# Performance work log

Hardware: AMD Instinct MI355X
Metric: run time of the kernel (lower is better)

## Reference

```python
import jax, jax.numpy as jnp
import numpy as np


def setup_inputs() -> dict:
    key = jax.random.key(0)
    ks = jax.random.split(key, 5)
    B, S, D = 4, 2048, 1024
    return {
        "query": jax.random.normal(ks[0], (B, S, D), dtype=jnp.float32),
        "value": jax.random.normal(ks[1], (B, S, D), dtype=jnp.float32),
        "Wq": jax.random.normal(ks[2], (D, D), dtype=jnp.float32) * 0.02,
        "Wk": jax.random.normal(ks[3], (D, D), dtype=jnp.float32) * 0.02,
        "Wv": jax.random.normal(ks[4], (D, D), dtype=jnp.float32) * 0.02,
        "num_heads": 16,
    }


def reference(query, value, Wq, Wk, Wv, num_heads):
    B, S, D = query.shape
    H = num_heads
    d = D // H
    # torch Linear: x @ W.T (no bias)
    Q = (query @ Wq.T).reshape(B, S, H, d)
    K = (value @ Wk.T).reshape(B, S, H, d)
    V = (value @ Wv.T).reshape(B, S, H, d)
    # Source scales by sqrt(hidden_size), not sqrt(head_dim)
    scale = 1.0 / jnp.sqrt(jnp.asarray(D, dtype=query.dtype))
    att = jnp.einsum("bqhd,bkhd->bhqk", Q, K) * scale  # [B,H,S,S]
    att = jax.nn.softmax(att, axis=-1)
    out = jnp.einsum("bhqk,bkhd->bqhd", att, V)  # [B,S,H,d]
    return out.reshape(B, S, D)
```

## Files before the change

### kernel.cpp

```cpp
#include <hip/hip_runtime.h>
#include <stdint.h>


typedef __attribute__((ext_vector_type(8))) short short8;
typedef __attribute__((ext_vector_type(4))) short s16x4;
typedef __attribute__((ext_vector_type(4))) float f32x4;

__device__ __forceinline__ unsigned short bf16_rne(float f) {
  union { float f; uint32_t u; } c; c.f = f;
  uint32_t u = c.u;
  return (unsigned short)((u + 0x7fffu + ((u >> 16) & 1u)) >> 16);
}

__device__ __forceinline__ f32x4 mfma_bf16(short8 a, short8 b, f32x4 c) {
  return __builtin_amdgcn_mfma_f32_16x16x32_bf16(a, b, c, 0, 0, 0);
}

#if __has_builtin(__builtin_amdgcn_mfma_f32_16x16x16bf16_1k)
__device__ __forceinline__ f32x4 mfma16(s16x4 a, s16x4 b, f32x4 c) {
  return __builtin_amdgcn_mfma_f32_16x16x16bf16_1k(a, b, c, 0, 0, 0);
}
#else
__device__ __forceinline__ f32x4 mfma16(s16x4 a, s16x4 b, f32x4 c) {
  asm volatile("v_mfma_f32_16x16x16_bf16 %0, %1, %2, %0"
               : "+v"(c) : "v"(a), "v"(b));
  return c;
}
#endif

#if __has_builtin(__builtin_amdgcn_exp2f)
#define EXP2F(x) __builtin_amdgcn_exp2f(x)
#else
#define EXP2F(x) exp2f(x)
#endif

__device__ __forceinline__ s16x4 cvtpk4(f32x4 v) {
  union { int i[2]; s16x4 s; } u;
  asm("v_cvt_pk_bf16_f32 %0, %1, %2" : "=v"(u.i[0]) : "v"(v[0]), "v"(v[1]));
  asm("v_cvt_pk_bf16_f32 %0, %1, %2" : "=v"(u.i[1]) : "v"(v[2]), "v"(v[3]));
  return u.s;
}

__device__ __forceinline__ void gload_lds16(const void* g, void* l) {
  __builtin_amdgcn_global_load_lds(
      (const __attribute__((address_space(1))) void*)g,
      (__attribute__((address_space(3))) void*)l,
      16, 0, 0);
}

__global__ void cvt_all(const float* __restrict__ q, const float* __restrict__ v,
                        const float* __restrict__ wq, const float* __restrict__ wk,
                        const float* __restrict__ wv,
                        unsigned short* __restrict__ xb, unsigned short* __restrict__ yb,
                        unsigned short* __restrict__ wqb, unsigned short* __restrict__ wkb,
                        unsigned short* __restrict__ wvb) {
  int blk = blockIdx.x;
  const float* src; unsigned short* dst; int off; float scale = 1.0f;
  if (blk < 8192)       { src = q;  dst = xb;  off = blk; }
  else if (blk < 16384) { src = v;  dst = yb;  off = blk - 8192; }
  else if (blk < 17408) { src = wq; dst = wqb; off = blk - 16384; scale = 0.04508422f; }
  else if (blk < 18432) { src = wk; dst = wkb; off = blk - 17408; }
  else                  { src = wv; dst = wvb; off = blk - 18432; }
  int i = (off * 256 + threadIdx.x) * 4;
  float4 x = *reinterpret_cast<const float4*>(src + i);
  ushort4 o;
  o.x = bf16_rne(x.x * scale); o.y = bf16_rne(x.y * scale);
  o.z = bf16_rne(x.z * scale); o.w = bf16_rne(x.w * scale);
  *reinterpret_cast<ushort4*>(dst + i) = o;
}

#define PG_K 1024

__global__ __launch_bounds__(256) void proj_gemm3(
    const unsigned short* __restrict__ xb, const unsigned short* __restrict__ yb,
    const unsigned short* __restrict__ wqb, const unsigned short* __restrict__ wkb,
    const unsigned short* __restrict__ wvb,
    unsigned short* __restrict__ qb, unsigned short* __restrict__ kb,
    unsigned short* __restrict__ vtb) {
  __shared__ char sA[128 * 128];
  __shared__ char sB[128 * 128];
  const int z = blockIdx.z;
  const unsigned short* A = (z == 0) ? xb : yb;
  const unsigned short* W = (z == 0) ? wqb : ((z == 1) ? wkb : wvb);
  unsigned short* outp = (z == 0) ? qb : ((z == 1) ? kb : vtb);
  const int mode = (z == 2) ? 1 : 0;

  const int t = threadIdx.x;
  const int wid = t >> 6;
  const int lane = t & 63;
  const int l15 = lane & 15, k16 = lane >> 4;
  const int bm = blockIdx.x * 128, bn = blockIdx.y * 128;
  const int wr = (wid >> 1) * 64, wc = (wid & 1) * 64;

  f32x4 acc[4][4];
#pragma unroll
  for (int m = 0; m < 4; ++m)
#pragma unroll
    for (int n = 0; n < 4; ++n) acc[m][n] = f32x4{0.f, 0.f, 0.f, 0.f};

  const int srow0 = t >> 3;
  const int cs = ((t & 7) * 16) ^ ((srow0 & 7) << 4);
  const char* gAr = (const char*)A + (size_t)(bm + srow0) * 2048 + cs;
  const char* gBr = (const char*)W + (size_t)(bn + srow0) * 2048 + cs;
  char* lA = sA + t * 16;
  char* lB = sB + t * 16;

  int afo[4][2], bfo[4][2];
#pragma unroll
  for (int m = 0; m < 4; ++m) {
    int ra = wr + m * 16 + l15, swa = (ra & 7) << 4;
    int rb = wc + m * 16 + l15, swb = (rb & 7) << 4;
#pragma unroll
    for (int h = 0; h < 2; ++h) {
      afo[m][h] = ra * 128 + ((h * 64 + k16 * 16) ^ swa);
      bfo[m][h] = rb * 128 + ((h * 64 + k16 * 16) ^ swb);
    }
  }

  for (int ks = 0; ks < 16; ++ks) {
    const int koff = ks * 128;
#pragma unroll
    for (int j = 0; j < 4; ++j) {
      gload_lds16(gAr + (size_t)j * 32 * 2048 + koff, lA + j * 4096);
      gload_lds16(gBr + (size_t)j * 32 * 2048 + koff, lB + j * 4096);
    }
    __syncthreads();
    short8 af[4][2], bfr[4][2];
#pragma unroll
    for (int m = 0; m < 4; ++m)
#pragma unroll
      for (int h = 0; h < 2; ++h) {
        af[m][h] = *reinterpret_cast<const short8*>(sA + afo[m][h]);
        bfr[m][h] = *reinterpret_cast<const short8*>(sB + bfo[m][h]);
      }
#pragma unroll
    for (int h = 0; h < 2; ++h)
#pragma unroll
      for (int m = 0; m < 4; ++m)
#pragma unroll
        for (int n = 0; n < 4; ++n)
          acc[m][n] = mfma_bf16(af[m][h], bfr[n][h], acc[m][n]);
    __syncthreads();
  }

#pragma unroll
  for (int m = 0; m < 4; ++m) {
#pragma unroll
    for (int n = 0; n < 4; ++n) {
#pragma unroll
      for (int j = 0; j < 4; ++j) {
        int row = bm + wr + m * 16 + k16 * 4 + j;
        int col = bn + wc + n * 16 + l15;
        int b = row >> 11, s = row & 2047;
        int h = col >> 6, jd = col & 63;
        int idx = (mode == 0) ? (((b * 16 + h) * 2048 + s) * 64 + jd)
                              : (((b * 16 + h) * 64 + jd) * 2048 + s);
        outp[idx] = bf16_rne(acc[m][n][j]);
      }
    }
  }
}

__global__ __launch_bounds__(256) void attn_lds(
    const unsigned short* __restrict__ qb, const unsigned short* __restrict__ kb,
    const unsigned short* __restrict__ vtb, float* __restrict__ out) {
  __shared__ char sK[2][8192];
  __shared__ char sV[2][8192];
  const int t = threadIdx.x;
  const int wid = t >> 6, lane = t & 63;
  const int l15 = lane & 15, k16 = lane >> 4;
  const int S = 2048;
  const int bid = blockIdx.x;
  const int xcd = bid & 7, slot = bid >> 3;
  const int bh = xcd * 8 + (slot >> 4);
  const int q0 = (slot & 15) * 128 + wid * 32;

  const unsigned short* Kh = kb + (size_t)bh * S * 64;
  const unsigned short* Vh = vtb + (size_t)bh * 64 * S;

  const int off0 = t * 16;
  const int off1 = 4096 + t * 16;
  const char* pk0 = (const char*)Kh + (off0 ^ (((off0 >> 7) & 7) << 4));
  const char* pk1 = (const char*)Kh + (off1 ^ (((off1 >> 7) & 7) << 4));
  const int vr0 = off0 >> 7, vc0 = off0 & 127;
  const int vr1 = off1 >> 7, vc1 = off1 & 127;
  const char* pv0 = (const char*)Vh + vr0 * (S * 2) + (vc0 ^ ((vr0 & 7) << 4));
  const char* pv1 = (const char*)Vh + vr1 * (S * 2) + (vc1 ^ ((vr1 & 7) << 4));

  short8 qf[2][2];
#pragma unroll
  for (int qt = 0; qt < 2; ++qt) {
    const unsigned short* qrow =
        qb + ((size_t)bh * S + q0 + qt * 16 + l15) * 64 + k16 * 8;
    qf[qt][0] = *reinterpret_cast<const short8*>(qrow);
    qf[qt][1] = *reinterpret_cast<const short8*>(qrow + 32);
  }

  int kfo[4][2], vfo[4][4];
#pragma unroll
  for (int n = 0; n < 4; ++n) {
    int row = n * 16 + l15, sw = (row & 7) << 4;
    kfo[n][0] = row * 128 + ((k16 * 16) ^ sw);
    kfo[n][1] = row * 128 + ((64 + k16 * 16) ^ sw);
  }
#pragma unroll
  for (int np = 0; np < 4; ++np) {
    int dv = np * 16 + l15, sw = (dv & 7) << 4;
#pragma unroll
    for (int kt = 0; kt < 4; ++kt)
      vfo[np][kt] = dv * 128 + ((kt * 32 + k16 * 8) ^ sw);
  }

  {
    char* lk = &sK[0][wid * 1024];
    char* lv = &sV[0][wid * 1024];
    gload_lds16(pk0, lk); gload_lds16(pk1, lk + 4096);
    gload_lds16(pv0, lv); gload_lds16(pv1, lv + 4096);
    pk0 += 8192; pk1 += 8192; pv0 += 128; pv1 += 128;
  }
  __syncthreads();

  f32x4 o[2][4];
  f32x4 lsum[2];
#pragma unroll
  for (int qt = 0; qt < 2; ++qt) {
    lsum[qt] = f32x4{0.f, 0.f, 0.f, 0.f};
#pragma unroll
    for (int np = 0; np < 4; ++np) o[qt][np] = f32x4{0.f, 0.f, 0.f, 0.f};
  }

  for (int tt = 0; tt < 32; ++tt) {
    const char* bK = sK[tt & 1];
    const char* bV = sV[tt & 1];
    if (tt < 31) {
      char* nk = &sK[(tt + 1) & 1][wid * 1024];
      char* nv = &sV[(tt + 1) & 1][wid * 1024];
      gload_lds16(pk0, nk); gload_lds16(pk1, nk + 4096);
      gload_lds16(pv0, nv); gload_lds16(pv1, nv + 4096);
      pk0 += 8192; pk1 += 8192; pv0 += 128; pv1 += 128;
    }

    f32x4 sa[2][4];
    __builtin_amdgcn_s_setprio(1);
#pragma unroll
    for (int n = 0; n < 4; ++n) {
      short8 kf0 = *reinterpret_cast<const short8*>(bK + kfo[n][0]);
      short8 kf1 = *reinterpret_cast<const short8*>(bK + kfo[n][1]);
#pragma unroll
      for (int qt = 0; qt < 2; ++qt) {
        f32x4 a = f32x4{0.f, 0.f, 0.f, 0.f};
        a = mfma_bf16(kf0, qf[qt][0], a);
        a = mfma_bf16(kf1, qf[qt][1], a);
        sa[qt][n] = a;
      }
    }
    __builtin_amdgcn_s_setprio(0);
    s16x4 pf[2][4];
#pragma unroll
    for (int qt = 0; qt < 2; ++qt)
#pragma unroll
      for (int n = 0; n < 4; ++n) {
#pragma unroll
        for (int r = 0; r < 4; ++r) sa[qt][n][r] = EXP2F(sa[qt][n][r]);
        lsum[qt] += sa[qt][n];
        pf[qt][n] = cvtpk4(sa[qt][n]);
      }
    __builtin_amdgcn_s_setprio(1);
#pragma unroll
    for (int np = 0; np < 4; ++np) {
      s16x4 vtx[4];
#pragma unroll
      for (int kt = 0; kt < 4; ++kt)
        vtx[kt] = *reinterpret_cast<const s16x4*>(bV + vfo[np][kt]);
#pragma unroll
      for (int qt = 0; qt < 2; ++qt)
#pragma unroll
        for (int n = 0; n < 4; ++n)
          o[qt][np] = mfma16(vtx[n], pf[qt][n], o[qt][np]);
    }
    __builtin_amdgcn_s_setprio(0);
    __syncthreads();
  }

  const int b = bh >> 4, h = bh & 15;
#pragma unroll
  for (int qt = 0; qt < 2; ++qt) {
    float l = (lsum[qt][0] + lsum[qt][1]) + (lsum[qt][2] + lsum[qt][3]);
    l += __shfl_xor(l, 16);
    l += __shfl_xor(l, 32);
    float inv = 1.0f / l;
    int s = q0 + qt * 16 + l15;
    float* orow = out + ((size_t)b * S + s) * 1024 + h * 64;
#pragma unroll
    for (int np = 0; np < 4; ++np) {
      float4 vv;
      vv.x = o[qt][np][0] * inv;
      vv.y = o[qt][np][1] * inv;
      vv.z = o[qt][np][2] * inv;
      vv.w = o[qt][np][3] * inv;
      *reinterpret_cast<float4*>(orow + np * 16 + k16 * 4) = vv;
    }
  }
}

extern "C" void kernel_launch(void* const* d_in, const int* in_sizes, int n_in,
                              void* d_out, int out_size, void* d_ws, size_t ws_size,
                              hipStream_t stream) {
  const float* q_f = (const float*)d_in[0];
  const float* v_f = (const float*)d_in[1];
  const float* wq_f = (const float*)d_in[2];
  const float* wk_f = (const float*)d_in[3];
  const float* wv_f = (const float*)d_in[4];
  float* out = (float*)d_out;

  unsigned short* xb  = (unsigned short*)d_ws;
  unsigned short* yb  = xb + 8388608;
  unsigned short* wqb = yb + 8388608;
  unsigned short* wkb = wqb + 1048576;
  unsigned short* wvb = wkb + 1048576;
  unsigned short* qb  = wvb + 1048576;
  unsigned short* kb  = qb + 8388608;
  unsigned short* vtb = kb + 8388608;

  cvt_all<<<19456, 256, 0, stream>>>(q_f, v_f, wq_f, wk_f, wv_f,
                                     xb, yb, wqb, wkb, wvb);

  dim3 gg(64, 8, 3);
  proj_gemm3<<<gg, 256, 0, stream>>>(xb, yb, wqb, wkb, wvb, qb, kb, vtb);

  attn_lds<<<1024, 256, 0, stream>>>(qb, kb, vtb, out);
}
```

Measured before the change: 287.2 us.

## Permute V^T storage so PV fragments load as two 16-byte LDS reads

The projection kernel now writes V transposed with a permutation of the sequence index inside each 64-wide block. Each lane's four 4-element V fragments become contiguous, so the attention loop fetches them with two 16-byte LDS reads per np instead of four 8-byte reads. The loop over query tiles is also restructured so each q-tile does QK, exp and PV in sequence, lowering live register pressure. The trade-off is that K and V fragments are reloaded from LDS once per q-tile.

```diff
diff --git a/kernel.cpp b/kernel.cpp
--- a/kernel.cpp
+++ b/kernel.cpp
@@ -153,8 +153,13 @@
         int col = bn + wc + n * 16 + l15;
         int b = row >> 11, s = row & 2047;
         int h = col >> 6, jd = col & 63;
-        int idx = (mode == 0) ? (((b * 16 + h) * 2048 + s) * 64 + jd)
-                              : (((b * 16 + h) * 64 + jd) * 2048 + s);
+        int idx;
+        if (mode == 0) {
+          idx = ((b * 16 + h) * 2048 + s) * 64 + jd;
+        } else {
+          int sp = (s & ~63) | ((s & 12) << 2) | ((s >> 2) & 12) | (s & 3);
+          idx = ((b * 16 + h) * 64 + jd) * 2048 + sp;
+        }
         outp[idx] = bf16_rne(acc[m][n][j]);
       }
     }
@@ -196,7 +201,7 @@
     qf[qt][1] = *reinterpret_cast<const short8*>(qrow + 32);
   }
 
-  int kfo[4][2], vfo[4][4];
+  int kfo[4][2], vfo[4][2];
 #pragma unroll
   for (int n = 0; n < 4; ++n) {
     int row = n * 16 + l15, sw = (row & 7) << 4;
@@ -206,9 +211,8 @@
 #pragma unroll
   for (int np = 0; np < 4; ++np) {
     int dv = np * 16 + l15, sw = (dv & 7) << 4;
-#pragma unroll
-    for (int kt = 0; kt < 4; ++kt)
-      vfo[np][kt] = dv * 128 + ((kt * 32 + k16 * 8) ^ sw);
+    vfo[np][0] = dv * 128 + ((k16 * 32) ^ sw);
+    vfo[np][1] = dv * 128 + ((k16 * 32 + 16) ^ sw);
   }
 
   {
@@ -240,45 +244,44 @@
       pk0 += 8192; pk1 += 8192; pv0 += 128; pv1 += 128;
     }
 
-    f32x4 sa[2][4];
-    __builtin_amdgcn_s_setprio(1);
-#pragma unroll
-    for (int n = 0; n < 4; ++n) {
-      short8 kf0 = *reinterpret_cast<const short8*>(bK + kfo[n][0]);
-      short8 kf1 = *reinterpret_cast<const short8*>(bK + kfo[n][1]);
-#pragma unroll
-      for (int qt = 0; qt < 2; ++qt) {
+#pragma unroll
+    for (int qt = 0; qt < 2; ++qt) {
+      f32x4 sa[4];
+      __builtin_amdgcn_s_setprio(1);
+#pragma unroll
+      for (int n = 0; n < 4; ++n) {
+        short8 kf0 = *reinterpret_cast<const short8*>(bK + kfo[n][0]);
+        short8 kf1 = *reinterpret_cast<const short8*>(bK + kfo[n][1]);
         f32x4 a = f32x4{0.f, 0.f, 0.f, 0.f};
         a = mfma_bf16(kf0, qf[qt][0], a);
         a = mfma_bf16(kf1, qf[qt][1], a);
-        sa[qt][n] = a;
-      }
-    }
-    __builtin_amdgcn_s_setprio(0);
-    s16x4 pf[2][4];
-#pragma unroll
-    for (int qt = 0; qt < 2; ++qt)
+        sa[n] = a;
+      }
+      __builtin_amdgcn_s_setprio(0);
+      s16x4 pf[4];
 #pragma unroll
       for (int n = 0; n < 4; ++n) {
 #pragma unroll
-        for (int r = 0; r < 4; ++r) sa[qt][n][r] = EXP2F(sa[qt][n][r]);
-        lsum[qt] += sa[qt][n];
-        pf[qt][n] = cvtpk4(sa[qt][n]);
-      }
-    __builtin_amdgcn_s_setprio(1);
-#pragma unroll
-    for (int np = 0; np < 4; ++np) {
-      s16x4 vtx[4];
-#pragma unroll
-      for (int kt = 0; kt < 4; ++kt)
-        vtx[kt] = *reinterpret_cast<const s16x4*>(bV + vfo[np][kt]);
-#pragma unroll
-      for (int qt = 0; qt < 2; ++qt)
-#pragma unroll
-        for (int n = 0; n < 4; ++n)
-          o[qt][np] = mfma16(vtx[n], pf[qt][n], o[qt][np]);
-    }
-    __builtin_amdgcn_s_setprio(0);
+        for (int r = 0; r < 4; ++r) sa[n][r] = EXP2F(sa[n][r]);
+        lsum[qt] += sa[n];
+        pf[n] = cvtpk4(sa[n]);
+      }
+      __builtin_amdgcn_s_setprio(1);
+#pragma unroll
+      for (int np = 0; np < 4; ++np) {
+        short8 w0 = *reinterpret_cast<const short8*>(bV + vfo[np][0]);
+        short8 w1 = *reinterpret_cast<const short8*>(bV + vfo[np][1]);
+        s16x4 v0 = __builtin_shufflevector(w0, w0, 0, 1, 2, 3);
+        s16x4 v1 = __builtin_shufflevector(w0, w0, 4, 5, 6, 7);
+        s16x4 v2 = __builtin_shufflevector(w1, w1, 0, 1, 2, 3);
+        s16x4 v3 = __builtin_shufflevector(w1, w1, 4, 5, 6, 7);
+        o[qt][np] = mfma16(v0, pf[0], o[qt][np]);
+        o[qt][np] = mfma16(v1, pf[1], o[qt][np]);
+        o[qt][np] = mfma16(v2, pf[2], o[qt][np]);
+        o[qt][np] = mfma16(v3, pf[3], o[qt][np]);
+      }
+      __builtin_amdgcn_s_setprio(0);
+    }
     __syncthreads();
   }
 
```

After: 286.7 us. About the same (-0.2%).
